# Kernel optimization log

Hardware: AMD Instinct MI355X
Metric: run time of the kernel (lower is better)

The kernel has to match this reference:

```python
import jax, jax.numpy as jnp
import numpy as np

B, T, IN, H, OUT = 16384, 60, 1, 50, 1


def setup_inputs() -> dict:
    key = jax.random.key(0)
    ks = jax.random.split(key, 7)
    s = 1.0 / np.sqrt(H)
    return {
        "input_seq": jax.random.normal(ks[0], (B, T, IN), dtype=jnp.float32),
        "w_ih": jax.random.uniform(ks[1], (4 * H, IN), jnp.float32, -s, s),
        "w_hh": jax.random.uniform(ks[2], (4 * H, H), jnp.float32, -s, s),
        "b_ih": jax.random.uniform(ks[3], (4 * H,), jnp.float32, -s, s),
        "b_hh": jax.random.uniform(ks[4], (4 * H,), jnp.float32, -s, s),
        "w_lin": jax.random.uniform(ks[5], (OUT, H * T), jnp.float32, -s, s),
        "b_lin": jax.random.uniform(ks[6], (OUT,), jnp.float32, -s, s),
    }


def reference(input_seq, w_ih, w_hh, b_ih, b_hh, w_lin, b_lin):
    # Precompute input projections for all timesteps: [T, B, 4H]
    x_proj = jnp.einsum('bti,gi->tbg', input_seq, w_ih) + b_ih + b_hh

    def step(carry, xp):
        h, c = carry
        gates = xp + h @ w_hh.T  # [B, 4H]
        i, f, g, o = jnp.split(gates, 4, axis=-1)  # PyTorch gate order
        i, f, o = jax.nn.sigmoid(i), jax.nn.sigmoid(f), jax.nn.sigmoid(o)
        g = jnp.tanh(g)
        c = f * c + i * g
        h = o * jnp.tanh(c)
        return (h, c), h

    h0 = jnp.zeros((input_seq.shape[0], H), dtype=input_seq.dtype)
    (_, _), hs = jax.lax.scan(step, (h0, h0), x_proj)  # hs: [T, B, H]
    lstm_out = jnp.transpose(hs, (1, 0, 2)).reshape(-1, H * T)  # [B, T*H]
    return lstm_out @ w_lin.T + b_lin
```

## Files before the change

kernel.cpp:

```cpp
#include <hip/hip_runtime.h>


namespace {
constexpr int TS = 60;
constexpr int NBW = 16;

typedef _Float16 half8 __attribute__((ext_vector_type(8)));
typedef _Float16 half4 __attribute__((ext_vector_type(4)));
typedef float f32x4 __attribute__((ext_vector_type(4)));

__device__ __forceinline__ float fexp2(float x) { return __builtin_amdgcn_exp2f(x); }
__device__ __forceinline__ float frcp(float x) { return __builtin_amdgcn_rcpf(x); }
__device__ __forceinline__ float sigm(float x) {
  return frcp(1.0f + fexp2(-1.4426950408889634f * x));
}
__device__ __forceinline__ float tanh_(float x) {
  return fmaf(-2.0f, frcp(1.0f + fexp2(2.8853900817779268f * x)), 1.0f);
}
__device__ __forceinline__ f32x4 mfma16(half8 a, half8 b, f32x4 c) {
  return __builtin_amdgcn_mfma_f32_16x16x32_f16(a, b, c, 0, 0, 0);
}
}

__global__ __launch_bounds__(256, 4) void lstm_w4(
    const float* __restrict__ x,
    const float* __restrict__ w_ih,
    const float* __restrict__ w_hh,
    const float* __restrict__ b_ih,
    const float* __restrict__ b_hh,
    const float* __restrict__ w_lin,
    const float* __restrict__ b_lin,
    float* __restrict__ out)
{
  __shared__ __align__(16) _Float16 HB[2][NBW * 64];
  __shared__ __align__(16) float WL[TS * 64];
  __shared__ __align__(16) float XL[TS * NBW];
  __shared__ float OB[4 * NBW];

  const int tid = threadIdx.x;
  const int lane = tid & 63;
  const int wv = tid >> 6;
  const int g = lane >> 4;
  const int cl = lane & 15;
  const long bbase = (long)blockIdx.x * NBW;

  for (int i = tid; i < TS * NBW; i += 256) {
    const int b = i / TS, t = i - b * TS;
    XL[t * NBW + b] = x[bbase * TS + i];
  }
  for (int i = tid; i < TS * 64; i += 256) {
    const int t = i >> 6, u = i & 63;
    WL[i] = (u < 50) ? w_lin[t * 50 + u] : 0.0f;
  }

  half8 A[4][2];
  {
    const int regA = cl & 3, gA = cl >> 2;
#pragma unroll
    for (int tau = 0; tau < 4; ++tau) {
      const int T = 4 * wv + tau;
      const int uA = 16 * gA + T;
      const int orig = regA * 50 + uA;
#pragma unroll
      for (int kc = 0; kc < 2; ++kc) {
        half8 frag;
        const int k0 = kc * 32 + 8 * g;
#pragma unroll
        for (int e = 0; e < 8; ++e) {
          const int k = k0 + e;
          float v = 0.0f;
          if (uA < 50) {
            if (k < 50) v = w_hh[orig * 50 + k];
            else if (k == 62) v = b_ih[orig] + b_hh[orig];
            else if (k == 63) v = w_ih[orig];
          }
          frag[e] = (_Float16)v;
        }
        A[tau][kc] = frag;
      }
    }
  }

  auto swzi = [&](int k) {
    return cl * 64 + ((((k >> 3) ^ (cl & 7)) << 3) | (k & 7));
  };
  const int rk0 = swzi(8 * g);
  const int rk1 = swzi(32 + 8 * g);
  const int wk = swzi(16 * g + 4 * wv);

  __syncthreads();

  {
    half4 z = {};
    if (wv == 3 && g == 3) {
      z[2] = (_Float16)1.0f;
      z[3] = (_Float16)XL[cl];
    }
    *(half4*)&HB[0][wk] = z;
  }
  __syncthreads();

  float c[4] = {0.f, 0.f, 0.f, 0.f};
  float oacc = 0.0f;

  auto step = [&](int t, const _Float16* RH, _Float16* WH) {
    const half8 B0 = *(const half8*)&RH[rk0];
    const half8 B1 = *(const half8*)&RH[rk1];
    f32x4 acc[4];
#pragma unroll
    for (int tau = 0; tau < 4; ++tau) {
      f32x4 a = {0.f, 0.f, 0.f, 0.f};
      a = mfma16(A[tau][0], B0, a);
      a = mfma16(A[tau][1], B1, a);
      acc[tau] = a;
    }
    const f32x4 wl = *(const f32x4*)&WL[t * 64 + 16 * g + 4 * wv];
    half4 hh;
#pragma unroll
    for (int tau = 0; tau < 4; ++tau) {
      const float ig = sigm(acc[tau][0]);
      const float fg = sigm(acc[tau][1]);
      const float gg = tanh_(acc[tau][2]);
      const float og = sigm(acc[tau][3]);
      const float cn = fmaf(fg, c[tau], ig * gg);
      c[tau] = cn;
      const float hn = og * tanh_(cn);
      oacc = fmaf(hn, wl[tau], oacc);
      hh[tau] = (_Float16)hn;
    }
    if (wv == 3 && g == 3) {
      hh[2] = (_Float16)1.0f;
      const int tn = (t + 1 < TS) ? (t + 1) : (TS - 1);
      hh[3] = (_Float16)XL[tn * NBW + cl];
    }
    *(half4*)&WH[wk] = hh;
    __syncthreads();
  };

#pragma unroll 1
  for (int t = 0; t < TS; t += 2) {
    step(t, HB[0], HB[1]);
    step(t + 1, HB[1], HB[0]);
  }

  oacc += __shfl_xor(oacc, 32);
  oacc += __shfl_xor(oacc, 16);
  if (lane < NBW) OB[wv * NBW + lane] = oacc;
  __syncthreads();
  if (tid < NBW) {
    float s = b_lin[0];
#pragma unroll
    for (int q = 0; q < 4; ++q) s += OB[q * NBW + tid];
    out[bbase + tid] = s;
  }
}

extern "C" void kernel_launch(void* const* d_in, const int* in_sizes, int n_in,
                              void* d_out, int out_size, void* d_ws, size_t ws_size,
                              hipStream_t stream) {
  const float* x     = (const float*)d_in[0];
  const float* w_ih  = (const float*)d_in[1];
  const float* w_hh  = (const float*)d_in[2];
  const float* b_ih  = (const float*)d_in[3];
  const float* b_hh  = (const float*)d_in[4];
  const float* w_lin = (const float*)d_in[5];
  const float* b_lin = (const float*)d_in[6];
  float* out = (float*)d_out;

  dim3 grid(16384 / NBW);
  dim3 block(256);
  lstm_w4<<<grid, block, 0, stream>>>(x, w_ih, w_hh, b_ih, b_hh, w_lin,
                                      b_lin, out);
}
```

Baseline: 98.51 us.

## Process two 16-sequence batch groups per block to reuse weight fragments

Each block now handles 32 sequences as two independent 16-column groups. The same register-resident w_hh fragments feed both groups' MFMAs, and the per-timestep barrier is shared between them. The two independent recurrences interleave, which can hide MFMA and transcendental latency and halves the number of blocks and barriers per sequence. In exchange, register use per thread roughly doubles for accumulators and state, the launch bound drops to 2 blocks per CU, and the grid halves, which may reduce occupancy.

```diff
diff --git a/kernel.cpp b/kernel.cpp
--- a/kernel.cpp
+++ b/kernel.cpp
@@ -3,7 +3,7 @@
 
 namespace {
 constexpr int TS = 60;
-constexpr int NBW = 16;
+constexpr int NBW = 32;
 
 typedef _Float16 half8 __attribute__((ext_vector_type(8)));
 typedef _Float16 half4 __attribute__((ext_vector_type(4)));
@@ -22,7 +22,7 @@
 }
 }
 
-__global__ __launch_bounds__(256, 4) void lstm_w4(
+__global__ __launch_bounds__(256, 2) void lstm_w4x2(
     const float* __restrict__ x,
     const float* __restrict__ w_ih,
     const float* __restrict__ w_hh,
@@ -32,10 +32,11 @@
     const float* __restrict__ b_lin,
     float* __restrict__ out)
 {
-  __shared__ __align__(16) _Float16 HB[2][NBW * 64];
+  __shared__ __align__(16) _Float16 HA[2][16 * 64];
+  __shared__ __align__(16) _Float16 HBf[2][16 * 64];
   __shared__ __align__(16) float WL[TS * 64];
   __shared__ __align__(16) float XL[TS * NBW];
-  __shared__ float OB[4 * NBW];
+  __shared__ float OB[4][2][16];
 
   const int tid = threadIdx.x;
   const int lane = tid & 63;
@@ -91,67 +92,102 @@
   __syncthreads();
 
   {
-    half4 z = {};
+    half4 z0 = {}, z1 = {};
     if (wv == 3 && g == 3) {
-      z[2] = (_Float16)1.0f;
-      z[3] = (_Float16)XL[cl];
-    }
-    *(half4*)&HB[0][wk] = z;
+      z0[2] = (_Float16)1.0f;
+      z0[3] = (_Float16)XL[cl];
+      z1[2] = (_Float16)1.0f;
+      z1[3] = (_Float16)XL[16 + cl];
+    }
+    *(half4*)&HA[0][wk] = z0;
+    *(half4*)&HBf[0][wk] = z1;
   }
   __syncthreads();
 
-  float c[4] = {0.f, 0.f, 0.f, 0.f};
-  float oacc = 0.0f;
-
-  auto step = [&](int t, const _Float16* RH, _Float16* WH) {
-    const half8 B0 = *(const half8*)&RH[rk0];
-    const half8 B1 = *(const half8*)&RH[rk1];
-    f32x4 acc[4];
+  float ca[4] = {0.f, 0.f, 0.f, 0.f};
+  float cb[4] = {0.f, 0.f, 0.f, 0.f};
+  float oa = 0.0f, ob = 0.0f;
+
+#pragma unroll 1
+  for (int t = 0; t < TS; ++t) {
+    const int p = t & 1;
+    const _Float16* RA = HA[p];
+    _Float16* WA = HA[p ^ 1];
+    const _Float16* RB = HBf[p];
+    _Float16* WB = HBf[p ^ 1];
+
+    const half8 Ba0 = *(const half8*)&RA[rk0];
+    const half8 Ba1 = *(const half8*)&RA[rk1];
+    const half8 Bb0 = *(const half8*)&RB[rk0];
+    const half8 Bb1 = *(const half8*)&RB[rk1];
+
+    f32x4 da[4], db[4];
 #pragma unroll
     for (int tau = 0; tau < 4; ++tau) {
       f32x4 a = {0.f, 0.f, 0.f, 0.f};
-      a = mfma16(A[tau][0], B0, a);
-      a = mfma16(A[tau][1], B1, a);
-      acc[tau] = a;
-    }
+      a = mfma16(A[tau][0], Ba0, a);
+      a = mfma16(A[tau][1], Ba1, a);
+      da[tau] = a;
+      f32x4 b = {0.f, 0.f, 0.f, 0.f};
+      b = mfma16(A[tau][0], Bb0, b);
+      b = mfma16(A[tau][1], Bb1, b);
+      db[tau] = b;
+    }
+
     const f32x4 wl = *(const f32x4*)&WL[t * 64 + 16 * g + 4 * wv];
-    half4 hh;
+    half4 ha, hb;
 #pragma unroll
     for (int tau = 0; tau < 4; ++tau) {
-      const float ig = sigm(acc[tau][0]);
-      const float fg = sigm(acc[tau][1]);
-      const float gg = tanh_(acc[tau][2]);
-      const float og = sigm(acc[tau][3]);
-      const float cn = fmaf(fg, c[tau], ig * gg);
-      c[tau] = cn;
-      const float hn = og * tanh_(cn);
-      oacc = fmaf(hn, wl[tau], oacc);
-      hh[tau] = (_Float16)hn;
+      {
+        const float ig = sigm(da[tau][0]);
+        const float fg = sigm(da[tau][1]);
+        const float gg = tanh_(da[tau][2]);
+        const float og = sigm(da[tau][3]);
+        const float cn = fmaf(fg, ca[tau], ig * gg);
+        ca[tau] = cn;
+        const float hn = og * tanh_(cn);
+        oa = fmaf(hn, wl[tau], oa);
+        ha[tau] = (_Float16)hn;
+      }
+      {
+        const float ig = sigm(db[tau][0]);
+        const float fg = sigm(db[tau][1]);
+        const float gg = tanh_(db[tau][2]);
+        const float og = sigm(db[tau][3]);
+        const float cn = fmaf(fg, cb[tau], ig * gg);
+        cb[tau] = cn;
+        const float hn = og * tanh_(cn);
+        ob = fmaf(hn, wl[tau], ob);
+        hb[tau] = (_Float16)hn;
+      }
     }
     if (wv == 3 && g == 3) {
-      hh[2] = (_Float16)1.0f;
       const int tn = (t + 1 < TS) ? (t + 1) : (TS - 1);
-      hh[3] = (_Float16)XL[tn * NBW + cl];
-    }
-    *(half4*)&WH[wk] = hh;
+      ha[2] = (_Float16)1.0f;
+      ha[3] = (_Float16)XL[tn * NBW + cl];
+      hb[2] = (_Float16)1.0f;
+      hb[3] = (_Float16)XL[tn * NBW + 16 + cl];
+    }
+    *(half4*)&WA[wk] = ha;
+    *(half4*)&WB[wk] = hb;
     __syncthreads();
-  };
-
-#pragma unroll 1
-  for (int t = 0; t < TS; t += 2) {
-    step(t, HB[0], HB[1]);
-    step(t + 1, HB[1], HB[0]);
-  }
-
-  oacc += __shfl_xor(oacc, 32);
-  oacc += __shfl_xor(oacc, 16);
-  if (lane < NBW) OB[wv * NBW + lane] = oacc;
+  }
+
+  oa += __shfl_xor(oa, 32);
+  oa += __shfl_xor(oa, 16);
+  ob += __shfl_xor(ob, 32);
+  ob += __shfl_xor(ob, 16);
+  if (lane < 16) {
+    OB[wv][0][lane] = oa;
+    OB[wv][1][lane] = ob;
+  }
   __syncthreads();
-  if (tid < NBW) {
+  if (tid < 32) {
+    const int grp = tid >> 4, b = tid & 15;
     float s = b_lin[0];
 #pragma unroll
-    for (int q = 0; q < 4; ++q) s += OB[q * NBW + tid];
-    out[bbase + tid] = s;
+    for (int q = 0; q < 4; ++q) s += OB[q][grp][b];
+    out[bbase + grp * 16 + b] = s;
   }
 }
 
@@ -169,6 +205,6 @@
 
   dim3 grid(16384 / NBW);
   dim3 block(256);
-  lstm_w4<<<grid, block, 0, stream>>>(x, w_ih, w_hh, b_ih, b_hh, w_lin,
-                                      b_lin, out);
-}
+  lstm_w4x2<<<grid, block, 0, stream>>>(x, w_ih, w_hh, b_ih, b_hh, w_lin,
+                                        b_lin, out);
+}
```

New measurement: 93.06 us. -5.5%, faster.
